# Performance work log

Hardware: AMD Instinct MI355X
Metric: run time of the kernel (lower is better)

Reference implementation:

```python
import jax, jax.numpy as jnp
import numpy as np
from jax import lax

K = 3          # kernel size
PAD = 1        # 'same' padding for k=3: (1,1,1,1)
STRIDE = 1
DIL = 1
OFFSET_SIZE = 2 * K * K  # deformable_groups=1


def setup_inputs() -> dict:
    key = jax.random.key(0)
    k1, k2, k3, k4 = jax.random.split(key, 4)
    B, H, W, C = 8, 64, 64, 256
    F = 256
    inputs = jax.random.normal(k1, (B, H, W, C), dtype=jnp.float32)
    # offset/mask branch conv: small weights so sampled offsets are modest
    om_kernel = jax.random.normal(k2, (K, K, C, OFFSET_SIZE * 3 // 2), dtype=jnp.float32) * 0.01
    om_bias = jnp.zeros((OFFSET_SIZE * 3 // 2,), dtype=jnp.float32)
    stdv = 1.0 / np.sqrt(K * K * C)
    kernel = jax.random.uniform(k3, (K * K * C, F), dtype=jnp.float32, minval=-stdv, maxval=stdv)
    bias = jax.random.normal(k4, (1, 1, 1, F), dtype=jnp.float32) * 0.01
    return {"inputs": inputs, "om_kernel": om_kernel, "om_bias": om_bias,
            "kernel": kernel, "bias": bias}


def _dcnv2(x, om_kernel, om_bias, kernel, bias):
    B, H, W, C = x.shape
    # offset/mask branch (same conv geometry as the deformable conv)
    om = lax.conv_general_dilated(
        x, om_kernel, window_strides=(STRIDE, STRIDE),
        padding=((PAD, PAD), (PAD, PAD)), rhs_dilation=(DIL, DIL),
        dimension_numbers=('NHWC', 'HWIO', 'NHWC')) + om_bias
    OH, OW = om.shape[1], om.shape[2]
    KK = K * K
    offset = om[..., :OFFSET_SIZE].reshape(B, OH, OW, KK, 2)  # (dy, dx) per kernel point
    mask = jax.nn.sigmoid(om[..., OFFSET_SIZE:]) * 2.0         # [B,OH,OW,KK]

    # base sampling grid per output pixel and kernel point
    kk = jnp.arange(KK)
    ky = (kk // K).astype(jnp.float32)
    kx = (kk % K).astype(jnp.float32)
    base_y = jnp.arange(OH, dtype=jnp.float32)[:, None] * STRIDE - PAD + ky[None, :] * DIL  # [OH,KK]
    base_x = jnp.arange(OW, dtype=jnp.float32)[:, None] * STRIDE - PAD + kx[None, :] * DIL  # [OW,KK]

    py = base_y[None, :, None, :] + offset[..., 0]  # [B,OH,OW,KK]
    px = base_x[None, None, :, :] + offset[..., 1]

    y0 = jnp.floor(py); x0 = jnp.floor(px)
    wy1 = py - y0; wy0 = 1.0 - wy1
    wx1 = px - x0; wx0 = 1.0 - wx1

    bi = jnp.arange(B)[:, None, None, None]

    def gather(yi, xi):
        # zero-padded bilinear corner fetch
        valid = (yi >= 0) & (yi <= H - 1) & (xi >= 0) & (xi <= W - 1)
        yc = jnp.clip(yi, 0, H - 1).astype(jnp.int32)
        xc = jnp.clip(xi, 0, W - 1).astype(jnp.int32)
        v = x[bi, yc, xc]  # [B,OH,OW,KK,C]
        return v * valid[..., None].astype(x.dtype)

    y1 = y0 + 1.0; x1 = x0 + 1.0
    cols = (gather(y0, x0) * (wy0 * wx0)[..., None]
            + gather(y0, x1) * (wy0 * wx1)[..., None]
            + gather(y1, x0) * (wy1 * wx0)[..., None]
            + gather(y1, x1) * (wy1 * wx1)[..., None])
    cols = cols * mask[..., None]  # modulation, [B,OH,OW,KK,C]

    out = cols.reshape(B, OH, OW, KK * C) @ kernel  # [B,OH,OW,F]
    return out + bias


def reference(inputs, om_kernel, om_bias, kernel, bias):
    return _dcnv2(inputs, om_kernel, om_bias, kernel, bias)
```

## Files before the change

### kernel.cpp

```cpp
#include <hip/hip_runtime.h>
#include <math.h>


#define BB 8
#define HH 64
#define WW 64
#define CIN 256
#define FF 256
#define KPTS 9
#define OCH 27
#define MT 64
#define KSTEPS 72

typedef _Float16 half8  __attribute__((ext_vector_type(8)));
typedef _Float16 half4v __attribute__((ext_vector_type(4)));
typedef float    floatx4 __attribute__((ext_vector_type(4)));

__device__ __forceinline__ int aoff(int m, int g) {
    return m * 32 + ((g ^ ((m >> 1) & 3)) << 3);
}

__device__ __forceinline__ half8 splat8(_Float16 v) {
    half8 r = {v, v, v, v, v, v, v, v};
    return r;
}

__global__ __launch_bounds__(256) void convert_x(const float* __restrict__ x,
                                                 _Float16* __restrict__ xh) {
    const size_t i = ((size_t)blockIdx.x * 256 + threadIdx.x) * 8;
    const floatx4 a = *(const floatx4*)(x + i);
    const floatx4 b = *(const floatx4*)(x + i + 4);
    half8 h;
    h[0] = (_Float16)a.x; h[1] = (_Float16)a.y; h[2] = (_Float16)a.z; h[3] = (_Float16)a.w;
    h[4] = (_Float16)b.x; h[5] = (_Float16)b.y; h[6] = (_Float16)b.z; h[7] = (_Float16)b.w;
    *(half8*)(xh + i) = h;
}

__global__ __launch_bounds__(256) void convert_wmat(const float* __restrict__ wmat,
                                                    _Float16* __restrict__ wsB) {
    const int kg = blockIdx.x;
    const int n  = threadIdx.x;
    half8 h;
    #pragma unroll
    for (int j = 0; j < 8; ++j)
        h[j] = (_Float16)wmat[(size_t)(kg * 8 + j) * FF + n];
    ((half8*)wsB)[(size_t)kg * FF + n] = h;
}

__global__ __launch_bounds__(256) void convert_omw(const float* __restrict__ omw,
                                                   _Float16* __restrict__ wsOM) {
    const int t = blockIdx.x * 256 + threadIdx.x;
    const int k = t >> 5, n = t & 31;
    const float v = (n < OCH) ? omw[k * OCH + n] : 0.f;
    wsOM[((size_t)(k >> 3) * 32 + n) * 8 + (k & 7)] = (_Float16)v;
}

template <bool F16X>
__global__ __launch_bounds__(512) void dcn_mfma2(
    const float* __restrict__ x,
    const _Float16* __restrict__ xh,
    const float* __restrict__ omb,
    const _Float16* __restrict__ wsB,
    const _Float16* __restrict__ wsOM,
    const float* __restrict__ bias,
    float* __restrict__ out)
{
    __shared__ _Float16 Ah0[MT * 32];
    __shared__ _Float16 Ah1[MT * 32];
    __shared__ float    om_s[MT][28];
    __shared__ half4v   cwS[MT][KPTS];
    __shared__ int4     caS[MT][KPTS];

    const int tid  = threadIdx.x;
    const int w    = tid >> 6;
    const int lane = tid & 63;
    const int q    = lane >> 4;
    const int lr   = lane & 15;
    const int g    = tid >> 8;
    const int st   = tid & 255;
    const int ms   = st >> 2;
    const int qc   = st & 3;

    const int p  = blockIdx.x;
    const int b  = p & 7;
    const int oh = p >> 3;
    const int pbase = (b * HH + oh) * WW;

    const half8* wsOM8 = (const half8*)wsOM;
    const half8* wsB8  = (const half8*)wsB;

    const int mt1 = w & 3;
    const int nt1 = w >> 2;
    floatx4 acc1 = {0.f, 0.f, 0.f, 0.f};

    auto load1 = [&](int sp) -> half8 {
        sp = sp < KSTEPS - 1 ? sp : KSTEPS - 1;
        const int kk = sp >> 3, cb = (sp & 7) << 5;
        const int ky = kk / 3, kx = kk - ky * 3;
        const int iy = oh - 1 + ky, ix = ms - 1 + kx;
        half8 v = {(_Float16)0, (_Float16)0, (_Float16)0, (_Float16)0,
                   (_Float16)0, (_Float16)0, (_Float16)0, (_Float16)0};
        if (iy >= 0 && iy < HH && ix >= 0 && ix < WW) {
            const int idx = ((b * HH + iy) * WW + ix) * CIN + cb + qc * 8;
            if constexpr (F16X) {
                v = *(const half8*)(xh + idx);
            } else {
                const floatx4 lo = *(const floatx4*)(x + idx);
                const floatx4 hi = *(const floatx4*)(x + idx + 4);
                v[0] = (_Float16)lo.x; v[1] = (_Float16)lo.y;
                v[2] = (_Float16)lo.z; v[3] = (_Float16)lo.w;
                v[4] = (_Float16)hi.x; v[5] = (_Float16)hi.y;
                v[6] = (_Float16)hi.z; v[7] = (_Float16)hi.w;
            }
        }
        return v;
    };
    auto loadB1 = [&](int sp) -> half8 {
        sp = sp < KSTEPS - 1 ? sp : KSTEPS - 1;
        return wsOM8[(sp * 4 + q) * 32 + nt1 * 16 + lr];
    };

    half8 vp1;
    half8 bo0, bo1;
    if (g == 0) {
        const half8 v0 = load1(0);
        *(half8*)(Ah0 + aoff(ms, qc)) = v0;
        vp1 = load1(2);
    } else {
        vp1 = load1(1);
    }
    bo0 = loadB1(0);

    for (int s = 0; s < KSTEPS; s += 2) {
        __syncthreads();
        if (g == 1) {
            *(half8*)(Ah1 + aoff(ms, qc)) = vp1;
            vp1 = load1(s + 3);
        }
        bo1 = loadB1(s + 1);
        {
            const half8 a = *(const half8*)(Ah0 + aoff(mt1 * 16 + lr, q));
            acc1 = __builtin_amdgcn_mfma_f32_16x16x32_f16(a, bo0, acc1, 0, 0, 0);
        }
        __syncthreads();
        if (g == 0) {
            *(half8*)(Ah0 + aoff(ms, qc)) = vp1;
            vp1 = load1(s + 4);
        }
        bo0 = loadB1(s + 2);
        {
            const half8 a = *(const half8*)(Ah1 + aoff(mt1 * 16 + lr, q));
            acc1 = __builtin_amdgcn_mfma_f32_16x16x32_f16(a, bo1, acc1, 0, 0, 0);
        }
    }
    {
        const int och = nt1 * 16 + lr;
        if (och < OCH) {
            const float ob = omb[och];
            #pragma unroll
            for (int reg = 0; reg < 4; ++reg) {
                const int m = mt1 * 16 + q * 4 + reg;
                om_s[m][och] = acc1[reg] + ob;
            }
        }
    }
    __syncthreads();

    for (int i = tid; i < MT * KPTS; i += 512) {
        const int m = i / KPTS, kk = i % KPTS;
        const int ky = kk / 3, kx = kk - ky * 3;
        const float dy = om_s[m][2 * kk];
        const float dx = om_s[m][2 * kk + 1];
        const float mask = 2.f / (1.f + __expf(-om_s[m][18 + kk]));
        const float py = (float)(oh - 1 + ky) + dy;
        const float px = (float)(m - 1 + kx) + dx;
        const float y0f = floorf(py), x0f = floorf(px);
        const float wy1 = py - y0f, wx1 = px - x0f;
        const float wy0 = 1.f - wy1, wx0 = 1.f - wx1;
        const int y0 = (int)y0f, x0 = (int)x0f;
        const int y1 = y0 + 1, x1 = x0 + 1;
        const bool vy0 = (y0 >= 0) && (y0 < HH);
        const bool vy1 = (y1 >= 0) && (y1 < HH);
        const bool vx0 = (x0 >= 0) && (x0 < WW);
        const bool vx1 = (x1 >= 0) && (x1 < WW);
        const int y0c = min(max(y0, 0), HH - 1), y1c = min(max(y1, 0), HH - 1);
        const int x0c = min(max(x0, 0), WW - 1), x1c = min(max(x1, 0), WW - 1);
        const int rb = b * HH;
        int4 ca;
        ca.x = ((rb + y0c) * WW + x0c) * CIN;
        ca.y = ((rb + y0c) * WW + x1c) * CIN;
        ca.z = ((rb + y1c) * WW + x0c) * CIN;
        ca.w = ((rb + y1c) * WW + x1c) * CIN;
        half4v cw;
        cw.x = (_Float16)((vy0 && vx0) ? mask * wy0 * wx0 : 0.f);
        cw.y = (_Float16)((vy0 && vx1) ? mask * wy0 * wx1 : 0.f);
        cw.z = (_Float16)((vy1 && vx0) ? mask * wy1 * wx0 : 0.f);
        cw.w = (_Float16)((vy1 && vx1) ? mask * wy1 * wx1 : 0.f);
        caS[m][kk] = ca;
        cwS[m][kk] = cw;
    }
    __syncthreads();

    floatx4 acc[4][2];
    #pragma unroll
    for (int mt = 0; mt < 4; ++mt)
        #pragma unroll
        for (int nt = 0; nt < 2; ++nt)
            acc[mt][nt] = (floatx4){0.f, 0.f, 0.f, 0.f};

    const int n0w = w * 32;

    half8   pc0, pc1, pc2, pc3;
    floatx4 fa0, fb0, fa1, fb1, fa2, fb2, fa3, fb3;
    half4v  pcw;

    auto pre2 = [&](int sp) {
        sp = sp < KSTEPS - 1 ? sp : KSTEPS - 1;
        const int kk = sp >> 3;
        const int co = ((sp & 7) << 5) + qc * 8;
        const int4 ca = caS[ms][kk];
        pcw = cwS[ms][kk];
        if constexpr (F16X) {
            pc0 = *(const half8*)(xh + ca.x + co);
            pc1 = *(const half8*)(xh + ca.y + co);
            pc2 = *(const half8*)(xh + ca.z + co);
            pc3 = *(const half8*)(xh + ca.w + co);
        } else {
            fa0 = *(const floatx4*)(x + ca.x + co); fb0 = *(const floatx4*)(x + ca.x + co + 4);
            fa1 = *(const floatx4*)(x + ca.y + co); fb1 = *(const floatx4*)(x + ca.y + co + 4);
            fa2 = *(const floatx4*)(x + ca.z + co); fb2 = *(const floatx4*)(x + ca.z + co + 4);
            fa3 = *(const floatx4*)(x + ca.w + co); fb3 = *(const floatx4*)(x + ca.w + co + 4);
        }
    };
    auto comb = [&]() -> half8 {
        if constexpr (F16X) {
            const half8 w0 = splat8(pcw.x), w1 = splat8(pcw.y);
            const half8 w2 = splat8(pcw.z), w3 = splat8(pcw.w);
            return pc0 * w0 + pc1 * w1 + pc2 * w2 + pc3 * w3;
        } else {
            const float w0 = (float)pcw.x, w1 = (float)pcw.y;
            const float w2 = (float)pcw.z, w3 = (float)pcw.w;
            const floatx4 lo = w0 * fa0 + w1 * fa1 + w2 * fa2 + w3 * fa3;
            const floatx4 hi = w0 * fb0 + w1 * fb1 + w2 * fb2 + w3 * fb3;
            half8 r;
            r[0] = (_Float16)lo.x; r[1] = (_Float16)lo.y;
            r[2] = (_Float16)lo.z; r[3] = (_Float16)lo.w;
            r[4] = (_Float16)hi.x; r[5] = (_Float16)hi.y;
            r[6] = (_Float16)hi.z; r[7] = (_Float16)hi.w;
            return r;
        }
    };

    half8 bPa[2], bPb[2];
    auto loadB2 = [&](int sp, half8 (&bP)[2]) {
        sp = sp < KSTEPS - 1 ? sp : KSTEPS - 1;
        #pragma unroll
        for (int nt = 0; nt < 2; ++nt)
            bP[nt] = wsB8[(size_t)(sp * 4 + q) * FF + n0w + nt * 16 + lr];
    };

    if (g == 0) {
        pre2(0);
        const half8 v0 = comb();
        *(half8*)(Ah0 + aoff(ms, qc)) = v0;
        pre2(2);
    } else {
        pre2(1);
    }
    loadB2(0, bPa);

    for (int s = 0; s < KSTEPS; s += 2) {
        __syncthreads();
        if (g == 1) {
            const half8 v = comb();
            *(half8*)(Ah1 + aoff(ms, qc)) = v;
            pre2(s + 3);
        }
        loadB2(s + 1, bPb);
        {
            half8 afr[4];
            #pragma unroll
            for (int mt = 0; mt < 4; ++mt)
                afr[mt] = *(const half8*)(Ah0 + aoff(mt * 16 + lr, q));
            #pragma unroll
            for (int nt = 0; nt < 2; ++nt)
                #pragma unroll
                for (int mt = 0; mt < 4; ++mt)
                    acc[mt][nt] = __builtin_amdgcn_mfma_f32_16x16x32_f16(afr[mt], bPa[nt], acc[mt][nt], 0, 0, 0);
        }
        __syncthreads();
        if (g == 0) {
            const half8 v = comb();
            *(half8*)(Ah0 + aoff(ms, qc)) = v;
            pre2(s + 4);
        }
        loadB2(s + 2, bPa);
        {
            half8 afr[4];
            #pragma unroll
            for (int mt = 0; mt < 4; ++mt)
                afr[mt] = *(const half8*)(Ah1 + aoff(mt * 16 + lr, q));
            #pragma unroll
            for (int nt = 0; nt < 2; ++nt)
                #pragma unroll
                for (int mt = 0; mt < 4; ++mt)
                    acc[mt][nt] = __builtin_amdgcn_mfma_f32_16x16x32_f16(afr[mt], bPb[nt], acc[mt][nt], 0, 0, 0);
        }
    }

    #pragma unroll
    for (int nt = 0; nt < 2; ++nt) {
        const int f = n0w + nt * 16 + lr;
        const float bv = bias[f];
        #pragma unroll
        for (int mt = 0; mt < 4; ++mt)
            #pragma unroll
            for (int reg = 0; reg < 4; ++reg) {
                const int m = mt * 16 + q * 4 + reg;
                out[(size_t)(pbase + m) * FF + f] = acc[mt][nt][reg] + bv;
            }
    }
}

#define MTILE 32
#define CHUNK 64
#define NCHUNK (CIN / CHUNK)

__global__ __launch_bounds__(256) void dcn_fused(
    const float* __restrict__ x, const float* __restrict__ omw,
    const float* __restrict__ omb, const float* __restrict__ wmat,
    const float* __restrict__ bias, float* __restrict__ out)
{
    __shared__ float A[CHUNK][MTILE + 1];
    __shared__ float om_s[MTILE][28];
    __shared__ float cw[MTILE][4];
    __shared__ int   ca[MTILE][4];

    const int tid = threadIdx.x;
    const int pbase = blockIdx.x * MTILE;
    const int ccid = tid & 63;
    const int mg2 = tid >> 6;
    const int och = tid & 31;
    const int mg1 = tid >> 5;
    float acc1[4] = {0.f, 0.f, 0.f, 0.f};

    for (int kk = 0; kk < KPTS; ++kk) {
        const int ky = kk / 3, kx = kk % 3;
        for (int ch = 0; ch < NCHUNK; ++ch) {
            const int cbase = ch * CHUNK;
            __syncthreads();
            #pragma unroll
            for (int i = 0; i < 8; ++i) {
                const int m = mg2 * 8 + i;
                const int pp = pbase + m;
                const int bb = pp >> 12, oh = (pp >> 6) & 63, ow = pp & 63;
                const int iy = oh - 1 + ky, ix = ow - 1 + kx;
                float v = 0.f;
                if (iy >= 0 && iy < HH && ix >= 0 && ix < WW)
                    v = x[((bb * HH + iy) * WW + ix) * CIN + cbase + ccid];
                A[ccid][m] = v;
            }
            __syncthreads();
            if (och < OCH) {
                for (int cc = 0; cc < CHUNK; ++cc) {
                    const float bv = omw[((kk * CIN) + cbase + cc) * OCH + och];
                    #pragma unroll
                    for (int i = 0; i < 4; ++i)
                        acc1[i] += A[cc][mg1 * 4 + i] * bv;
                }
            }
        }
    }
    __syncthreads();
    if (och < OCH) {
        const float ob = omb[och];
        #pragma unroll
        for (int i = 0; i < 4; ++i)
            om_s[mg1 * 4 + i][och] = acc1[i] + ob;
    }
    __syncthreads();

    const int f4 = (tid & 63) * 4;
    const int mgc = tid >> 6;
    float acc[8][4];
    #pragma unroll
    for (int j = 0; j < 8; ++j)
        #pragma unroll
        for (int i = 0; i < 4; ++i) acc[j][i] = 0.f;

    for (int kk = 0; kk < KPTS; ++kk) {
        if (tid < MTILE) {
            const int m = tid;
            const int pp = pbase + m;
            const int bb = pp >> 12, oh = (pp >> 6) & 63, ow = pp & 63;
            const int ky = kk / 3, kx = kk % 3;
            const float dy = om_s[m][2 * kk];
            const float dx = om_s[m][2 * kk + 1];
            const float mask = 2.f / (1.f + __expf(-om_s[m][18 + kk]));
            const float py = (float)(oh - 1 + ky) + dy;
            const float px = (float)(ow - 1 + kx) + dx;
            const float y0f = floorf(py), x0f = floorf(px);
            const float wy1 = py - y0f, wx1 = px - x0f;
            const float wy0 = 1.f - wy1, wx0 = 1.f - wx1;
            const int y0 = (int)y0f, x0 = (int)x0f;
            const int y1 = y0 + 1, x1 = x0 + 1;
            const bool vy0 = (y0 >= 0) && (y0 < HH);
            const bool vy1 = (y1 >= 0) && (y1 < HH);
            const bool vx0 = (x0 >= 0) && (x0 < WW);
            const bool vx1 = (x1 >= 0) && (x1 < WW);
            const int y0c = min(max(y0, 0), HH - 1), y1c = min(max(y1, 0), HH - 1);
            const int x0c = min(max(x0, 0), WW - 1), x1c = min(max(x1, 0), WW - 1);
            const int rb = bb * HH;
            ca[m][0] = ((rb + y0c) * WW + x0c) * CIN;
            ca[m][1] = ((rb + y0c) * WW + x1c) * CIN;
            ca[m][2] = ((rb + y1c) * WW + x0c) * CIN;
            ca[m][3] = ((rb + y1c) * WW + x1c) * CIN;
            cw[m][0] = (vy0 && vx0) ? mask * wy0 * wx0 : 0.f;
            cw[m][1] = (vy0 && vx1) ? mask * wy0 * wx1 : 0.f;
            cw[m][2] = (vy1 && vx0) ? mask * wy1 * wx0 : 0.f;
            cw[m][3] = (vy1 && vx1) ? mask * wy1 * wx1 : 0.f;
        }
        for (int ch = 0; ch < NCHUNK; ++ch) {
            const int cbase = ch * CHUNK;
            __syncthreads();
            #pragma unroll
            for (int i = 0; i < 8; ++i) {
                const int m = mg2 * 8 + i;
                const int cidx = cbase + ccid;
                const float v = cw[m][0] * x[ca[m][0] + cidx]
                              + cw[m][1] * x[ca[m][1] + cidx]
                              + cw[m][2] * x[ca[m][2] + cidx]
                              + cw[m][3] * x[ca[m][3] + cidx];
                A[ccid][m] = v;
            }
            __syncthreads();
            const float* brow = wmat + (size_t)(kk * CIN + cbase) * FF + f4;
            for (int cc = 0; cc < CHUNK; ++cc) {
                const float4 bv = *(const float4*)(brow + cc * FF);
                #pragma unroll
                for (int j = 0; j < 8; ++j) {
                    const float a = A[cc][mgc * 8 + j];
                    acc[j][0] += a * bv.x;
                    acc[j][1] += a * bv.y;
                    acc[j][2] += a * bv.z;
                    acc[j][3] += a * bv.w;
                }
            }
        }
    }

    const float4 bb4 = *(const float4*)(bias + f4);
    #pragma unroll
    for (int j = 0; j < 8; ++j) {
        const int m = mgc * 8 + j;
        const int pp = pbase + m;
        float4 o;
        o.x = acc[j][0] + bb4.x;
        o.y = acc[j][1] + bb4.y;
        o.z = acc[j][2] + bb4.z;
        o.w = acc[j][3] + bb4.w;
        *(float4*)(out + (size_t)pp * FF + f4) = o;
    }
}

extern "C" void kernel_launch(void* const* d_in, const int* in_sizes, int n_in,
                              void* d_out, int out_size, void* d_ws, size_t ws_size,
                              hipStream_t stream) {
    const float* x    = (const float*)d_in[0];
    const float* omw  = (const float*)d_in[1];
    const float* omb  = (const float*)d_in[2];
    const float* wmat = (const float*)d_in[3];
    const float* bias = (const float*)d_in[4];
    float* out = (float*)d_out;

    const size_t needB  = (size_t)2304 * FF * sizeof(_Float16);
    const size_t needOM = (size_t)288 * 32 * 8 * sizeof(_Float16);
    const size_t needX  = (size_t)BB * HH * WW * CIN * sizeof(_Float16);

    if (ws_size >= needB + needOM + needX) {
        _Float16* wsB  = (_Float16*)d_ws;
        _Float16* wsOM = (_Float16*)((char*)d_ws + needB);
        _Float16* xh   = (_Float16*)((char*)d_ws + needB + needOM);
        convert_x<<<(BB * HH * WW * CIN) / (256 * 8), 256, 0, stream>>>(x, xh);
        convert_wmat<<<288, 256, 0, stream>>>(wmat, wsB);
        convert_omw<<<288, 256, 0, stream>>>(omw, wsOM);
        dcn_mfma2<true><<<BB * HH, 512, 0, stream>>>(x, xh, omb, wsB, wsOM, bias, out);
    } else if (ws_size >= needB + needOM) {
        _Float16* wsB  = (_Float16*)d_ws;
        _Float16* wsOM = (_Float16*)((char*)d_ws + needB);
        convert_wmat<<<288, 256, 0, stream>>>(wmat, wsB);
        convert_omw<<<288, 256, 0, stream>>>(omw, wsOM);
        dcn_mfma2<false><<<BB * HH, 512, 0, stream>>>(x, nullptr, omb, wsB, wsOM, bias, out);
    } else {
        const int nblocks = (BB * HH * WW) / MTILE;
        dcn_fused<<<nblocks, 256, 0, stream>>>(x, omw, omb, wmat, bias, out);
    }
}
```

Before: 170.1 us.

## Widen K-step to 64 channels, use all threads per stage, fuse conversion kernels

Doubles the K-chunk per pipeline stage from 32 to 64 channels, so every one of the 512 threads stages A data each step instead of half the block alternating. This halves the number of barrier-separated steps and issues two MFMAs per tile per stage. It also widens the LDS swizzle, adds a min-blocks launch bound, and merges the three fp16 conversion kernels into one launch to cut launch overhead. The cost is more registers for the extra prefetched B fragments and gather loads, which could limit occupancy.

```diff
diff --git a/kernel.cpp b/kernel.cpp
--- a/kernel.cpp
+++ b/kernel.cpp
@@ -10,14 +10,14 @@
 #define KPTS 9
 #define OCH 27
 #define MT 64
-#define KSTEPS 72
+#define NS2 36
 
 typedef _Float16 half8  __attribute__((ext_vector_type(8)));
 typedef _Float16 half4v __attribute__((ext_vector_type(4)));
 typedef float    floatx4 __attribute__((ext_vector_type(4)));
 
 __device__ __forceinline__ int aoff(int m, int g) {
-    return m * 32 + ((g ^ ((m >> 1) & 3)) << 3);
+    return m * 64 + ((g ^ (m & 7)) << 3);
 }
 
 __device__ __forceinline__ half8 splat8(_Float16 v) {
@@ -25,38 +25,40 @@
     return r;
 }
 
-__global__ __launch_bounds__(256) void convert_x(const float* __restrict__ x,
-                                                 _Float16* __restrict__ xh) {
-    const size_t i = ((size_t)blockIdx.x * 256 + threadIdx.x) * 8;
-    const floatx4 a = *(const floatx4*)(x + i);
-    const floatx4 b = *(const floatx4*)(x + i + 4);
-    half8 h;
-    h[0] = (_Float16)a.x; h[1] = (_Float16)a.y; h[2] = (_Float16)a.z; h[3] = (_Float16)a.w;
-    h[4] = (_Float16)b.x; h[5] = (_Float16)b.y; h[6] = (_Float16)b.z; h[7] = (_Float16)b.w;
-    *(half8*)(xh + i) = h;
-}
-
-__global__ __launch_bounds__(256) void convert_wmat(const float* __restrict__ wmat,
-                                                    _Float16* __restrict__ wsB) {
-    const int kg = blockIdx.x;
-    const int n  = threadIdx.x;
-    half8 h;
-    #pragma unroll
-    for (int j = 0; j < 8; ++j)
-        h[j] = (_Float16)wmat[(size_t)(kg * 8 + j) * FF + n];
-    ((half8*)wsB)[(size_t)kg * FF + n] = h;
-}
-
-__global__ __launch_bounds__(256) void convert_omw(const float* __restrict__ omw,
-                                                   _Float16* __restrict__ wsOM) {
-    const int t = blockIdx.x * 256 + threadIdx.x;
-    const int k = t >> 5, n = t & 31;
-    const float v = (n < OCH) ? omw[k * OCH + n] : 0.f;
-    wsOM[((size_t)(k >> 3) * 32 + n) * 8 + (k & 7)] = (_Float16)v;
+#define XBLK 4096
+__global__ __launch_bounds__(256) void convert_all(
+    const float* __restrict__ x, const float* __restrict__ wmat,
+    const float* __restrict__ omw,
+    _Float16* __restrict__ xh, _Float16* __restrict__ wsB, _Float16* __restrict__ wsOM)
+{
+    const int bid = blockIdx.x;
+    if (bid < XBLK) {
+        if (xh == nullptr) return;
+        const size_t i = ((size_t)bid * 256 + threadIdx.x) * 8;
+        const floatx4 a = *(const floatx4*)(x + i);
+        const floatx4 b = *(const floatx4*)(x + i + 4);
+        half8 h;
+        h[0] = (_Float16)a.x; h[1] = (_Float16)a.y; h[2] = (_Float16)a.z; h[3] = (_Float16)a.w;
+        h[4] = (_Float16)b.x; h[5] = (_Float16)b.y; h[6] = (_Float16)b.z; h[7] = (_Float16)b.w;
+        *(half8*)(xh + i) = h;
+    } else if (bid < XBLK + 288) {
+        const int kg = bid - XBLK;
+        const int n  = threadIdx.x;
+        half8 h;
+        #pragma unroll
+        for (int j = 0; j < 8; ++j)
+            h[j] = (_Float16)wmat[(size_t)(kg * 8 + j) * FF + n];
+        ((half8*)wsB)[(size_t)kg * FF + n] = h;
+    } else {
+        const int t = (bid - XBLK - 288) * 256 + threadIdx.x;
+        const int k = t >> 5, n = t & 31;
+        const float v = (n < OCH) ? omw[k * OCH + n] : 0.f;
+        wsOM[((size_t)(k >> 3) * 32 + n) * 8 + (k & 7)] = (_Float16)v;
+    }
 }
 
 template <bool F16X>
-__global__ __launch_bounds__(512) void dcn_mfma2(
+__global__ __launch_bounds__(512, 4) void dcn_mfma3(
     const float* __restrict__ x,
     const _Float16* __restrict__ xh,
     const float* __restrict__ omb,
@@ -65,8 +67,8 @@
     const float* __restrict__ bias,
     float* __restrict__ out)
 {
-    __shared__ _Float16 Ah0[MT * 32];
-    __shared__ _Float16 Ah1[MT * 32];
+    __shared__ _Float16 Ah0[MT * 64];
+    __shared__ _Float16 Ah1[MT * 64];
     __shared__ float    om_s[MT][28];
     __shared__ half4v   cwS[MT][KPTS];
     __shared__ int4     caS[MT][KPTS];
@@ -76,10 +78,8 @@
     const int lane = tid & 63;
     const int q    = lane >> 4;
     const int lr   = lane & 15;
-    const int g    = tid >> 8;
-    const int st   = tid & 255;
-    const int ms   = st >> 2;
-    const int qc   = st & 3;
+    const int ms   = tid >> 3;
+    const int qc   = tid & 7;
 
     const int p  = blockIdx.x;
     const int b  = p & 7;
@@ -94,8 +94,8 @@
     floatx4 acc1 = {0.f, 0.f, 0.f, 0.f};
 
     auto load1 = [&](int sp) -> half8 {
-        sp = sp < KSTEPS - 1 ? sp : KSTEPS - 1;
-        const int kk = sp >> 3, cb = (sp & 7) << 5;
+        sp = sp < NS2 - 1 ? sp : NS2 - 1;
+        const int kk = sp >> 2, cb = (sp & 3) << 6;
         const int ky = kk / 3, kx = kk - ky * 3;
         const int iy = oh - 1 + ky, ix = ms - 1 + kx;
         half8 v = {(_Float16)0, (_Float16)0, (_Float16)0, (_Float16)0,
@@ -115,42 +115,40 @@
         }
         return v;
     };
-    auto loadB1 = [&](int sp) -> half8 {
-        sp = sp < KSTEPS - 1 ? sp : KSTEPS - 1;
-        return wsOM8[(sp * 4 + q) * 32 + nt1 * 16 + lr];
+    auto loadB1 = [&](int sp, half8& b0, half8& b1) {
+        sp = sp < NS2 - 1 ? sp : NS2 - 1;
+        b0 = wsOM8[(sp * 8 + q) * 32 + nt1 * 16 + lr];
+        b1 = wsOM8[(sp * 8 + 4 + q) * 32 + nt1 * 16 + lr];
     };
 
-    half8 vp1;
-    half8 bo0, bo1;
-    if (g == 0) {
+    half8 vp;
+    half8 bo00, bo01, bo10, bo11;
+    {
         const half8 v0 = load1(0);
         *(half8*)(Ah0 + aoff(ms, qc)) = v0;
-        vp1 = load1(2);
-    } else {
-        vp1 = load1(1);
-    }
-    bo0 = loadB1(0);
-
-    for (int s = 0; s < KSTEPS; s += 2) {
+        vp = load1(1);
+        loadB1(0, bo00, bo01);
+    }
+    for (int s = 0; s < NS2; s += 2) {
         __syncthreads();
-        if (g == 1) {
-            *(half8*)(Ah1 + aoff(ms, qc)) = vp1;
-            vp1 = load1(s + 3);
-        }
-        bo1 = loadB1(s + 1);
+        *(half8*)(Ah1 + aoff(ms, qc)) = vp;
+        vp = load1(s + 2);
+        loadB1(s + 1, bo10, bo11);
         {
-            const half8 a = *(const half8*)(Ah0 + aoff(mt1 * 16 + lr, q));
-            acc1 = __builtin_amdgcn_mfma_f32_16x16x32_f16(a, bo0, acc1, 0, 0, 0);
+            const half8 a0 = *(const half8*)(Ah0 + aoff(mt1 * 16 + lr, q));
+            const half8 a1 = *(const half8*)(Ah0 + aoff(mt1 * 16 + lr, 4 + q));
+            acc1 = __builtin_amdgcn_mfma_f32_16x16x32_f16(a0, bo00, acc1, 0, 0, 0);
+            acc1 = __builtin_amdgcn_mfma_f32_16x16x32_f16(a1, bo01, acc1, 0, 0, 0);
         }
         __syncthreads();
-        if (g == 0) {
-            *(half8*)(Ah0 + aoff(ms, qc)) = vp1;
-            vp1 = load1(s + 4);
-        }
-        bo0 = loadB1(s + 2);
+        *(half8*)(Ah0 + aoff(ms, qc)) = vp;
+        vp = load1(s + 3);
+        loadB1(s + 2, bo00, bo01);
         {
-            const half8 a = *(const half8*)(Ah1 + aoff(mt1 * 16 + lr, q));
-            acc1 = __builtin_amdgcn_mfma_f32_16x16x32_f16(a, bo1, acc1, 0, 0, 0);
+            const half8 a0 = *(const half8*)(Ah1 + aoff(mt1 * 16 + lr, q));
+            const half8 a1 = *(const half8*)(Ah1 + aoff(mt1 * 16 + lr, 4 + q));
+            acc1 = __builtin_amdgcn_mfma_f32_16x16x32_f16(a0, bo10, acc1, 0, 0, 0);
+            acc1 = __builtin_amdgcn_mfma_f32_16x16x32_f16(a1, bo11, acc1, 0, 0, 0);
         }
     }
     {
@@ -215,9 +213,9 @@
     half4v  pcw;
 
     auto pre2 = [&](int sp) {
-        sp = sp < KSTEPS - 1 ? sp : KSTEPS - 1;
-        const int kk = sp >> 3;
-        const int co = ((sp & 7) << 5) + qc * 8;
+        sp = sp < NS2 - 1 ? sp : NS2 - 1;
+        const int kk = sp >> 2;
+        const int co = ((sp & 3) << 6) + qc * 8;
         const int4 ca = caS[ms][kk];
         pcw = cwS[ms][kk];
         if constexpr (F16X) {
@@ -251,60 +249,61 @@
         }
     };
 
-    half8 bPa[2], bPb[2];
-    auto loadB2 = [&](int sp, half8 (&bP)[2]) {
-        sp = sp < KSTEPS - 1 ? sp : KSTEPS - 1;
-        #pragma unroll
-        for (int nt = 0; nt < 2; ++nt)
-            bP[nt] = wsB8[(size_t)(sp * 4 + q) * FF + n0w + nt * 16 + lr];
+    half8 bPa[2][2], bPb[2][2];
+    auto loadB2 = [&](int sp, half8 (&bP)[2][2]) {
+        sp = sp < NS2 - 1 ? sp : NS2 - 1;
+        #pragma unroll
+        for (int kh = 0; kh < 2; ++kh)
+            #pragma unroll
+            for (int nt = 0; nt < 2; ++nt)
+                bP[kh][nt] = wsB8[(size_t)(sp * 8 + kh * 4 + q) * FF + n0w + nt * 16 + lr];
     };
 
-    if (g == 0) {
+    {
         pre2(0);
         const half8 v0 = comb();
         *(half8*)(Ah0 + aoff(ms, qc)) = v0;
-        pre2(2);
-    } else {
         pre2(1);
-    }
-    loadB2(0, bPa);
-
-    for (int s = 0; s < KSTEPS; s += 2) {
+        loadB2(0, bPa);
+    }
+    for (int s = 0; s < NS2; s += 2) {
         __syncthreads();
-        if (g == 1) {
+        {
             const half8 v = comb();
             *(half8*)(Ah1 + aoff(ms, qc)) = v;
-            pre2(s + 3);
-        }
+        }
+        pre2(s + 2);
         loadB2(s + 1, bPb);
-        {
+        #pragma unroll
+        for (int kh = 0; kh < 2; ++kh) {
             half8 afr[4];
             #pragma unroll
             for (int mt = 0; mt < 4; ++mt)
-                afr[mt] = *(const half8*)(Ah0 + aoff(mt * 16 + lr, q));
+                afr[mt] = *(const half8*)(Ah0 + aoff(mt * 16 + lr, kh * 4 + q));
             #pragma unroll
             for (int nt = 0; nt < 2; ++nt)
                 #pragma unroll
                 for (int mt = 0; mt < 4; ++mt)
-                    acc[mt][nt] = __builtin_amdgcn_mfma_f32_16x16x32_f16(afr[mt], bPa[nt], acc[mt][nt], 0, 0, 0);
+                    acc[mt][nt] = __builtin_amdgcn_mfma_f32_16x16x32_f16(afr[mt], bPa[kh][nt], acc[mt][nt], 0, 0, 0);
         }
         __syncthreads();
-        if (g == 0) {
+        {
             const half8 v = comb();
             *(half8*)(Ah0 + aoff(ms, qc)) = v;
-            pre2(s + 4);
-        }
+        }
+        pre2(s + 3);
         loadB2(s + 2, bPa);
-        {
+        #pragma unroll
+        for (int kh = 0; kh < 2; ++kh) {
             half8 afr[4];
             #pragma unroll
             for (int mt = 0; mt < 4; ++mt)
-                afr[mt] = *(const half8*)(Ah1 + aoff(mt * 16 + lr, q));
+                afr[mt] = *(const half8*)(Ah1 + aoff(mt * 16 + lr, kh * 4 + q));
             #pragma unroll
             for (int nt = 0; nt < 2; ++nt)
                 #pragma unroll
                 for (int mt = 0; mt < 4; ++mt)
-                    acc[mt][nt] = __builtin_amdgcn_mfma_f32_16x16x32_f16(afr[mt], bPb[nt], acc[mt][nt], 0, 0, 0);
+                    acc[mt][nt] = __builtin_amdgcn_mfma_f32_16x16x32_f16(afr[mt], bPb[kh][nt], acc[mt][nt], 0, 0, 0);
         }
     }
 
@@ -481,16 +480,13 @@
         _Float16* wsB  = (_Float16*)d_ws;
         _Float16* wsOM = (_Float16*)((char*)d_ws + needB);
         _Float16* xh   = (_Float16*)((char*)d_ws + needB + needOM);
-        convert_x<<<(BB * HH * WW * CIN) / (256 * 8), 256, 0, stream>>>(x, xh);
-        convert_wmat<<<288, 256, 0, stream>>>(wmat, wsB);
-        convert_omw<<<288, 256, 0, stream>>>(omw, wsOM);
-        dcn_mfma2<true><<<BB * HH, 512, 0, stream>>>(x, xh, omb, wsB, wsOM, bias, out);
+        convert_all<<<XBLK + 288 + 288, 256, 0, stream>>>(x, wmat, omw, xh, wsB, wsOM);
+        dcn_mfma3<true><<<BB * HH, 512, 0, stream>>>(x, xh, omb, wsB, wsOM, bias, out);
     } else if (ws_size >= needB + needOM) {
         _Float16* wsB  = (_Float16*)d_ws;
         _Float16* wsOM = (_Float16*)((char*)d_ws + needB);
-        convert_wmat<<<288, 256, 0, stream>>>(wmat, wsB);
-        convert_omw<<<288, 256, 0, stream>>>(omw, wsOM);
-        dcn_mfma2<false><<<BB * HH, 512, 0, stream>>>(x, nullptr, omb, wsB, wsOM, bias, out);
+        convert_all<<<XBLK + 288 + 288, 256, 0, stream>>>(x, wmat, omw, nullptr, wsB, wsOM);
+        dcn_mfma3<false><<<BB * HH, 512, 0, stream>>>(x, nullptr, omb, wsB, wsOM, bias, out);
     } else {
         const int nblocks = (BB * HH * WW) / MTILE;
         dcn_fused<<<nblocks, 256, 0, stream>>>(x, omw, omb, wmat, bias, out);
```

Result: faster. 163.1 us (-4.1%).
